# Kernel tuning notes

Hardware: AMD Instinct MI355X
Metric: run time of the kernel (lower is better)

## Reference

```python
import jax, jax.numpy as jnp
import numpy as np

N_LOC = 500000
N_CAT = 5000
N_EDGES = 2000000
LOC_DIM = 128
CAT_DIM = 128
INITRANGE = 0.1
NEG_SLOPE = 0.2


def setup_inputs() -> dict:
    key = jax.random.key(0)
    k1, k2, k3, k4 = jax.random.split(key, 4)
    loc_emb = jax.random.normal(k1, (N_LOC, LOC_DIM), dtype=jnp.float32)
    # loc_to_cat Linear params, init per init_weights(): uniform(-0.1, 0.1) weight, zero bias
    W = jax.random.uniform(k2, (CAT_DIM, LOC_DIM), dtype=jnp.float32,
                           minval=-INITRANGE, maxval=INITRANGE)
    b = jnp.zeros((CAT_DIM,), dtype=jnp.float32)
    edge_src = jax.random.randint(k3, (N_EDGES,), 0, N_LOC, dtype=jnp.int64)
    edge_dst = jax.random.randint(k4, (N_EDGES,), 0, N_CAT, dtype=jnp.int64)
    return {"loc_emb": loc_emb, "W": W, "b": b,
            "edge_src": edge_src, "edge_dst": edge_dst}


def reference(loc_emb, W, b, edge_src, edge_dst):
    # copy_u('f','m') + sum('m','in') across all canonical etypes, combined with 'sum':
    # gather source (loc) features along edges, segment-sum into cat nodes.
    msg = loc_emb[edge_src]                                   # [E, loc_dim]
    agg = jax.ops.segment_sum(msg, edge_dst, num_segments=N_CAT)  # [n_cat, loc_dim]
    # loc_to_cat linear + LeakyReLU(0.2)
    cat_emb = jax.nn.leaky_relu(agg @ W.T + b, negative_slope=NEG_SLOPE)
    return cat_emb
```

## Files before the change

### kernel.cpp

```cpp
#include <hip/hip_runtime.h>

#define N_LOC   500000
#define N_CAT   5000
#define N_EDGES 2000000
#define DIM     128
#define NEG_SLOPE 0.2f
#define PAD     5008
#define NB      256
#define EPB     ((N_EDGES + NB - 1) / NB)


__launch_bounds__(1024)
__global__ void blockhist_kernel(const int* __restrict__ edst, int* __restrict__ rank,
                                 int* __restrict__ bhist) {
    __shared__ int lh[N_CAT];
    int b = blockIdx.x, t = threadIdx.x;
    for (int c = t; c < N_CAT; c += 1024) lh[c] = 0;
    __syncthreads();
    int s = b * EPB;
    int e = min(s + EPB, N_EDGES);
    for (int i = s + t; i < e; i += 1024)
        rank[i] = atomicAdd(&lh[edst[i]], 1);
    __syncthreads();
    for (int c = t; c < N_CAT; c += 1024)
        bhist[(size_t)b * N_CAT + c] = lh[c];
}

__launch_bounds__(256)
__global__ void blockscan_kernel(int* __restrict__ bhist, int* __restrict__ tot) {
    int c = blockIdx.x * 256 + threadIdx.x;
    if (c >= N_CAT) return;
    int run = 0;
    for (int b0 = 0; b0 < NB; b0 += 8) {
        int v0 = bhist[(size_t)(b0 + 0) * N_CAT + c];
        int v1 = bhist[(size_t)(b0 + 1) * N_CAT + c];
        int v2 = bhist[(size_t)(b0 + 2) * N_CAT + c];
        int v3 = bhist[(size_t)(b0 + 3) * N_CAT + c];
        int v4 = bhist[(size_t)(b0 + 4) * N_CAT + c];
        int v5 = bhist[(size_t)(b0 + 5) * N_CAT + c];
        int v6 = bhist[(size_t)(b0 + 6) * N_CAT + c];
        int v7 = bhist[(size_t)(b0 + 7) * N_CAT + c];
        bhist[(size_t)(b0 + 0) * N_CAT + c] = run; run += v0;
        bhist[(size_t)(b0 + 1) * N_CAT + c] = run; run += v1;
        bhist[(size_t)(b0 + 2) * N_CAT + c] = run; run += v2;
        bhist[(size_t)(b0 + 3) * N_CAT + c] = run; run += v3;
        bhist[(size_t)(b0 + 4) * N_CAT + c] = run; run += v4;
        bhist[(size_t)(b0 + 5) * N_CAT + c] = run; run += v5;
        bhist[(size_t)(b0 + 6) * N_CAT + c] = run; run += v6;
        bhist[(size_t)(b0 + 7) * N_CAT + c] = run; run += v7;
    }
    tot[c] = run;
}

__launch_bounds__(1024)
__global__ void scan_kernel(const int* __restrict__ cnt, int* __restrict__ offsets) {
    __shared__ int wsum[16];
    __shared__ int woff[16];
    __shared__ int total_s;
    __shared__ int running_s;
    int t = threadIdx.x;
    int lane = t & 63, w = t >> 6;
    if (t == 0) { running_s = 0; offsets[0] = 0; }
    __syncthreads();
    for (int base = 0; base < N_CAT; base += 1024) {
        int i = base + t;
        int v = (i < N_CAT) ? cnt[i] : 0;
        int incl = v;
        #pragma unroll
        for (int off = 1; off < 64; off <<= 1) {
            int x = __shfl_up(incl, off, 64);
            if (lane >= off) incl += x;
        }
        if (lane == 63) wsum[w] = incl;
        __syncthreads();
        if (w == 0 && lane < 16) {
            int s = wsum[lane];
            int e = s;
            #pragma unroll
            for (int off = 1; off < 16; off <<= 1) {
                int x = __shfl_up(e, off, 64);
                if (lane >= off) e += x;
            }
            woff[lane] = e - s;
            if (lane == 15) total_s = e;
        }
        __syncthreads();
        int run = running_s;
        if (i < N_CAT) offsets[i + 1] = run + woff[w] + incl;
        __syncthreads();
        if (t == 0) running_s = run + total_s;
        __syncthreads();
    }
}

__global__ void fill2_kernel(const int* __restrict__ esrc, const int* __restrict__ edst,
                             const int* __restrict__ rank, const int* __restrict__ offsets,
                             const int* __restrict__ bhist, int* __restrict__ csr_src) {
    int i = blockIdx.x * blockDim.x + threadIdx.x;
    if (i < N_EDGES) {
        int c = edst[i];
        int b = i / EPB;
        csr_src[offsets[c] + bhist[(size_t)b * N_CAT + c] + rank[i]] = esrc[i];
    }
}

__global__ void transpose_kernel(const float* __restrict__ W, float* __restrict__ WT) {
    int j = blockIdx.x;
    int k = threadIdx.x;
    WT[k * DIM + j] = W[j * DIM + k];
}

__launch_bounds__(256)
__global__ void agg_fused_kernel(const float* __restrict__ loc, const int* __restrict__ csr_src,
                                 const int* __restrict__ offsets, const float* __restrict__ WT,
                                 const float* __restrict__ bias, float* __restrict__ out) {
    __shared__ float4 sacc[256];
    __shared__ float  srow[DIM];
    int c = blockIdx.x;
    int t = threadIdx.x;
    int g = t >> 5;
    int l = t & 31;
    int beg = offsets[c];
    int end = offsets[c + 1];
    int cnt = end - beg;
    int per = (cnt + 7) >> 3;
    int gbeg = beg + g * per;
    int gend = min(gbeg + per, end);

    float4 a0 = make_float4(0.f, 0.f, 0.f, 0.f);
    float4 a1 = make_float4(0.f, 0.f, 0.f, 0.f);
    float4 a2 = make_float4(0.f, 0.f, 0.f, 0.f);
    float4 a3 = make_float4(0.f, 0.f, 0.f, 0.f);
    int e = gbeg;
    for (; e + 4 <= gend; e += 4) {
        int s0 = csr_src[e + 0];
        int s1 = csr_src[e + 1];
        int s2 = csr_src[e + 2];
        int s3 = csr_src[e + 3];
        float4 v0 = ((const float4*)(loc + (size_t)s0 * DIM))[l];
        float4 v1 = ((const float4*)(loc + (size_t)s1 * DIM))[l];
        float4 v2 = ((const float4*)(loc + (size_t)s2 * DIM))[l];
        float4 v3 = ((const float4*)(loc + (size_t)s3 * DIM))[l];
        a0.x += v0.x; a0.y += v0.y; a0.z += v0.z; a0.w += v0.w;
        a1.x += v1.x; a1.y += v1.y; a1.z += v1.z; a1.w += v1.w;
        a2.x += v2.x; a2.y += v2.y; a2.z += v2.z; a2.w += v2.w;
        a3.x += v3.x; a3.y += v3.y; a3.z += v3.z; a3.w += v3.w;
    }
    for (; e < gend; ++e) {
        int s = csr_src[e];
        float4 v = ((const float4*)(loc + (size_t)s * DIM))[l];
        a0.x += v.x; a0.y += v.y; a0.z += v.z; a0.w += v.w;
    }
    float4 acc = make_float4((a0.x + a1.x) + (a2.x + a3.x),
                             (a0.y + a1.y) + (a2.y + a3.y),
                             (a0.z + a1.z) + (a2.z + a3.z),
                             (a0.w + a1.w) + (a2.w + a3.w));
    sacc[t] = acc;
    __syncthreads();
    if (t < 128) {
        float4 a = sacc[t], b = sacc[t + 128];
        sacc[t] = make_float4(a.x + b.x, a.y + b.y, a.z + b.z, a.w + b.w);
    }
    __syncthreads();
    if (t < 64) {
        float4 a = sacc[t], b = sacc[t + 64];
        sacc[t] = make_float4(a.x + b.x, a.y + b.y, a.z + b.z, a.w + b.w);
    }
    __syncthreads();
    if (t < 32) {
        float4 a = sacc[t], b = sacc[t + 32];
        srow[4 * t + 0] = a.x + b.x;
        srow[4 * t + 1] = a.y + b.y;
        srow[4 * t + 2] = a.z + b.z;
        srow[4 * t + 3] = a.w + b.w;
    }
    __syncthreads();
    int j = t & 127;
    int h = t >> 7;
    float m0 = 0.f, m1 = 0.f, m2 = 0.f, m3 = 0.f;
    int k0 = h * 64;
    #pragma unroll 4
    for (int k = 0; k < 64; k += 4) {
        m0 += WT[(k0 + k + 0) * DIM + j] * srow[k0 + k + 0];
        m1 += WT[(k0 + k + 1) * DIM + j] * srow[k0 + k + 1];
        m2 += WT[(k0 + k + 2) * DIM + j] * srow[k0 + k + 2];
        m3 += WT[(k0 + k + 3) * DIM + j] * srow[k0 + k + 3];
    }
    float* sred = (float*)sacc;
    sred[t] = (m0 + m1) + (m2 + m3);
    __syncthreads();
    if (t < 128) {
        float v = sred[t] + sred[t + 128] + bias[t];
        v = v > 0.f ? v : NEG_SLOPE * v;
        out[(size_t)c * DIM + t] = v;
    }
}


__global__ void hist_rank_kernel(const int* __restrict__ dst, int* __restrict__ cnt,
                                 int* __restrict__ rank, int n) {
    int i = blockIdx.x * blockDim.x + threadIdx.x;
    if (i < n) rank[i] = atomicAdd(&cnt[dst[i]], 1);
}

__global__ void fill_rank_kernel(const int* __restrict__ src, const int* __restrict__ dst,
                                 const int* __restrict__ rank, const int* __restrict__ offsets,
                                 int* __restrict__ csr_src, int n) {
    int i = blockIdx.x * blockDim.x + threadIdx.x;
    if (i < n) csr_src[offsets[dst[i]] + rank[i]] = src[i];
}

__global__ void zero_kernel(float* p, int n) {
    int i = blockIdx.x * blockDim.x + threadIdx.x;
    if (i < n) p[i] = 0.f;
}

__launch_bounds__(128)
__global__ void scatter_atomic_kernel(const float* __restrict__ loc, const int* __restrict__ src,
                                      const int* __restrict__ dst, float* __restrict__ agg) {
    int e = blockIdx.x;
    int d = threadIdx.x;
    int s = src[e];
    int c = dst[e];
    atomicAdd(&agg[(size_t)c * DIM + d], loc[(size_t)s * DIM + d]);
}

#define CATS_PER_BLOCK 8
__launch_bounds__(256)
__global__ void gemm_lrelu_kernel(const float* __restrict__ agg, const float* __restrict__ W,
                                  const float* __restrict__ b, float* __restrict__ out) {
    __shared__ float sW[DIM * 129];
    __shared__ float sA[CATS_PER_BLOCK * DIM];
    int t = threadIdx.x;
    int cbase = blockIdx.x * CATS_PER_BLOCK;
    for (int i = t; i < DIM * DIM; i += 256) {
        int j = i >> 7, k = i & 127;
        sW[j * 129 + k] = W[i];
    }
    for (int i = t; i < CATS_PER_BLOCK * DIM; i += 256) {
        sA[i] = agg[(size_t)cbase * DIM + i];
    }
    __syncthreads();
    int j = t & 127;
    int cc = t >> 7;
    float acc0 = 0.f, acc1 = 0.f, acc2 = 0.f, acc3 = 0.f;
    for (int k = 0; k < DIM; ++k) {
        float w = sW[j * 129 + k];
        acc0 += w * sA[(cc + 0) * DIM + k];
        acc1 += w * sA[(cc + 2) * DIM + k];
        acc2 += w * sA[(cc + 4) * DIM + k];
        acc3 += w * sA[(cc + 6) * DIM + k];
    }
    float bj = b[j];
    float r0 = acc0 + bj, r1 = acc1 + bj, r2 = acc2 + bj, r3 = acc3 + bj;
    r0 = r0 > 0.f ? r0 : NEG_SLOPE * r0;
    r1 = r1 > 0.f ? r1 : NEG_SLOPE * r1;
    r2 = r2 > 0.f ? r2 : NEG_SLOPE * r2;
    r3 = r3 > 0.f ? r3 : NEG_SLOPE * r3;
    out[(size_t)(cbase + cc + 0) * DIM + j] = r0;
    out[(size_t)(cbase + cc + 2) * DIM + j] = r1;
    out[(size_t)(cbase + cc + 4) * DIM + j] = r2;
    out[(size_t)(cbase + cc + 6) * DIM + j] = r3;
}

extern "C" void kernel_launch(void* const* d_in, const int* in_sizes, int n_in,
                              void* d_out, int out_size, void* d_ws, size_t ws_size,
                              hipStream_t stream) {
    const float* loc  = (const float*)d_in[0];
    const float* W    = (const float*)d_in[1];
    const float* bias = (const float*)d_in[2];
    const int*   esrc = (const int*)d_in[3];
    const int*   edst = (const int*)d_in[4];
    float* out = (float*)d_out;

    const int threads = 256;
    const int eblocks = (N_EDGES + threads - 1) / threads;

    size_t need_cs   = ((size_t)2 * N_EDGES + (size_t)NB * N_CAT + 2 * PAD + DIM * DIM) * sizeof(int);
    size_t need_rank = ((size_t)2 * N_EDGES + 2 * PAD + DIM * DIM) * sizeof(int);

    if (ws_size >= need_cs) {
        int*   rank    = (int*)d_ws;
        int*   csr_src = rank + N_EDGES;
        int*   bhist   = csr_src + N_EDGES;
        int*   tot     = bhist + (size_t)NB * N_CAT;
        int*   offsets = tot + PAD;
        float* WT      = (float*)(offsets + PAD);

        transpose_kernel<<<DIM, DIM, 0, stream>>>(W, WT);
        blockhist_kernel<<<NB, 1024, 0, stream>>>(edst, rank, bhist);
        blockscan_kernel<<<(N_CAT + 255) / 256, 256, 0, stream>>>(bhist, tot);
        scan_kernel<<<1, 1024, 0, stream>>>(tot, offsets);
        fill2_kernel<<<eblocks, threads, 0, stream>>>(esrc, edst, rank, offsets, bhist, csr_src);
        agg_fused_kernel<<<N_CAT, 256, 0, stream>>>(loc, csr_src, offsets, WT, bias, out);
    } else if (ws_size >= need_rank) {
        int* counts  = (int*)d_ws;
        int* offsets = counts + PAD;
        float* WT    = (float*)(offsets + PAD);
        int* rank    = (int*)(WT + DIM * DIM);
        int* csr_src = rank + N_EDGES;

        hipMemsetAsync(counts, 0, (size_t)PAD * sizeof(int), stream);
        transpose_kernel<<<DIM, DIM, 0, stream>>>(W, WT);
        hist_rank_kernel<<<eblocks, threads, 0, stream>>>(edst, counts, rank, N_EDGES);
        scan_kernel<<<1, 1024, 0, stream>>>(counts, offsets);
        fill_rank_kernel<<<eblocks, threads, 0, stream>>>(esrc, edst, rank, offsets, csr_src, N_EDGES);
        agg_fused_kernel<<<N_CAT, 256, 0, stream>>>(loc, csr_src, offsets, WT, bias, out);
    } else {
        int n = N_CAT * DIM;
        zero_kernel<<<(n + 255) / 256, 256, 0, stream>>>(out, n);
        scatter_atomic_kernel<<<N_EDGES, DIM, 0, stream>>>(loc, esrc, edst, out);
        gemm_lrelu_kernel<<<N_CAT / CATS_PER_BLOCK, 256, 0, stream>>>(out, W, bias, out);
    }
}
```

Baseline: 504.1 us.

## Fold weight transpose into histogram kernel, vectorize edge passes, deepen gather unroll

```diff
diff --git a/kernel.cpp b/kernel.cpp
--- a/kernel.cpp
+++ b/kernel.cpp
@@ -6,21 +6,40 @@
 #define DIM     128
 #define NEG_SLOPE 0.2f
 #define PAD     5008
-#define NB      256
-#define EPB     ((N_EDGES + NB - 1) / NB)
-
+#define NB      128
+#define EPB     15628
 
 __launch_bounds__(1024)
-__global__ void blockhist_kernel(const int* __restrict__ edst, int* __restrict__ rank,
+__global__ void blockhist_kernel(const int* __restrict__ edst, const float* __restrict__ W,
+                                 float* __restrict__ WT, int* __restrict__ rank,
                                  int* __restrict__ bhist) {
+    int b = blockIdx.x, t = threadIdx.x;
+    if (b == NB) {
+        for (int i = t; i < DIM * DIM; i += 1024) {
+            int j = i >> 7, k = i & 127;
+            WT[k * DIM + j] = W[j * DIM + k];
+        }
+        return;
+    }
     __shared__ int lh[N_CAT];
-    int b = blockIdx.x, t = threadIdx.x;
     for (int c = t; c < N_CAT; c += 1024) lh[c] = 0;
     __syncthreads();
     int s = b * EPB;
     int e = min(s + EPB, N_EDGES);
-    for (int i = s + t; i < e; i += 1024)
-        rank[i] = atomicAdd(&lh[edst[i]], 1);
+    int i = s + 4 * t;
+    for (; i + 4 <= e; i += 4096) {
+        int4 d = *(const int4*)(edst + i);
+        int4 r;
+        r.x = atomicAdd(&lh[d.x], 1);
+        r.y = atomicAdd(&lh[d.y], 1);
+        r.z = atomicAdd(&lh[d.z], 1);
+        r.w = atomicAdd(&lh[d.w], 1);
+        *(int4*)(rank + i) = r;
+    }
+    if (i < e) {
+        int lim = min(i + 4, e);
+        for (int j = i; j < lim; ++j) rank[j] = atomicAdd(&lh[edst[j]], 1);
+    }
     __syncthreads();
     for (int c = t; c < N_CAT; c += 1024)
         bhist[(size_t)b * N_CAT + c] = lh[c];
@@ -56,8 +75,7 @@
 __global__ void scan_kernel(const int* __restrict__ cnt, int* __restrict__ offsets) {
     __shared__ int wsum[16];
     __shared__ int woff[16];
-    __shared__ int total_s;
-    __shared__ int running_s;
+    __shared__ int total_s, running_s;
     int t = threadIdx.x;
     int lane = t & 63, w = t >> 6;
     if (t == 0) { running_s = 0; offsets[0] = 0; }
@@ -96,18 +114,23 @@
 __global__ void fill2_kernel(const int* __restrict__ esrc, const int* __restrict__ edst,
                              const int* __restrict__ rank, const int* __restrict__ offsets,
                              const int* __restrict__ bhist, int* __restrict__ csr_src) {
-    int i = blockIdx.x * blockDim.x + threadIdx.x;
-    if (i < N_EDGES) {
-        int c = edst[i];
-        int b = i / EPB;
-        csr_src[offsets[c] + bhist[(size_t)b * N_CAT + c] + rank[i]] = esrc[i];
-    }
-}
-
-__global__ void transpose_kernel(const float* __restrict__ W, float* __restrict__ WT) {
-    int j = blockIdx.x;
-    int k = threadIdx.x;
-    WT[k * DIM + j] = W[j * DIM + k];
+    int i4 = (blockIdx.x * blockDim.x + threadIdx.x) * 4;
+    if (i4 + 4 <= N_EDGES) {
+        int4 c = *(const int4*)(edst + i4);
+        int4 s = *(const int4*)(esrc + i4);
+        int4 r = *(const int4*)(rank + i4);
+        size_t bb = (size_t)(i4 / EPB) * N_CAT;
+        csr_src[offsets[c.x] + bhist[bb + c.x] + r.x] = s.x;
+        csr_src[offsets[c.y] + bhist[bb + c.y] + r.y] = s.y;
+        csr_src[offsets[c.z] + bhist[bb + c.z] + r.z] = s.z;
+        csr_src[offsets[c.w] + bhist[bb + c.w] + r.w] = s.w;
+    } else {
+        for (int i = i4; i < N_EDGES; ++i) {
+            int c = edst[i];
+            size_t bb = (size_t)(i / EPB) * N_CAT;
+            csr_src[offsets[c] + bhist[bb + c] + rank[i]] = esrc[i];
+        }
+    }
 }
 
 __launch_bounds__(256)
@@ -132,11 +155,28 @@
     float4 a2 = make_float4(0.f, 0.f, 0.f, 0.f);
     float4 a3 = make_float4(0.f, 0.f, 0.f, 0.f);
     int e = gbeg;
+    for (; e + 8 <= gend; e += 8) {
+        int s0 = csr_src[e + 0], s1 = csr_src[e + 1], s2 = csr_src[e + 2], s3 = csr_src[e + 3];
+        int s4 = csr_src[e + 4], s5 = csr_src[e + 5], s6 = csr_src[e + 6], s7 = csr_src[e + 7];
+        float4 v0 = ((const float4*)(loc + (size_t)s0 * DIM))[l];
+        float4 v1 = ((const float4*)(loc + (size_t)s1 * DIM))[l];
+        float4 v2 = ((const float4*)(loc + (size_t)s2 * DIM))[l];
+        float4 v3 = ((const float4*)(loc + (size_t)s3 * DIM))[l];
+        float4 v4 = ((const float4*)(loc + (size_t)s4 * DIM))[l];
+        float4 v5 = ((const float4*)(loc + (size_t)s5 * DIM))[l];
+        float4 v6 = ((const float4*)(loc + (size_t)s6 * DIM))[l];
+        float4 v7 = ((const float4*)(loc + (size_t)s7 * DIM))[l];
+        a0.x += v0.x; a0.y += v0.y; a0.z += v0.z; a0.w += v0.w;
+        a1.x += v1.x; a1.y += v1.y; a1.z += v1.z; a1.w += v1.w;
+        a2.x += v2.x; a2.y += v2.y; a2.z += v2.z; a2.w += v2.w;
+        a3.x += v3.x; a3.y += v3.y; a3.z += v3.z; a3.w += v3.w;
+        a0.x += v4.x; a0.y += v4.y; a0.z += v4.z; a0.w += v4.w;
+        a1.x += v5.x; a1.y += v5.y; a1.z += v5.z; a1.w += v5.w;
+        a2.x += v6.x; a2.y += v6.y; a2.z += v6.z; a2.w += v6.w;
+        a3.x += v7.x; a3.y += v7.y; a3.z += v7.z; a3.w += v7.w;
+    }
     for (; e + 4 <= gend; e += 4) {
-        int s0 = csr_src[e + 0];
-        int s1 = csr_src[e + 1];
-        int s2 = csr_src[e + 2];
-        int s3 = csr_src[e + 3];
+        int s0 = csr_src[e + 0], s1 = csr_src[e + 1], s2 = csr_src[e + 2], s3 = csr_src[e + 3];
         float4 v0 = ((const float4*)(loc + (size_t)s0 * DIM))[l];
         float4 v1 = ((const float4*)(loc + (size_t)s1 * DIM))[l];
         float4 v2 = ((const float4*)(loc + (size_t)s2 * DIM))[l];
@@ -210,6 +250,12 @@
     if (i < n) csr_src[offsets[dst[i]] + rank[i]] = src[i];
 }
 
+__global__ void transpose_kernel(const float* __restrict__ W, float* __restrict__ WT) {
+    int j = blockIdx.x;
+    int k = threadIdx.x;
+    WT[k * DIM + j] = W[j * DIM + k];
+}
+
 __global__ void zero_kernel(float* p, int n) {
     int i = blockIdx.x * blockDim.x + threadIdx.x;
     if (i < n) p[i] = 0.f;
@@ -220,9 +266,7 @@
                                       const int* __restrict__ dst, float* __restrict__ agg) {
     int e = blockIdx.x;
     int d = threadIdx.x;
-    int s = src[e];
-    int c = dst[e];
-    atomicAdd(&agg[(size_t)c * DIM + d], loc[(size_t)s * DIM + d]);
+    atomicAdd(&agg[(size_t)dst[e] * DIM + d], loc[(size_t)src[e] * DIM + d]);
 }
 
 #define CATS_PER_BLOCK 8
@@ -237,9 +281,8 @@
         int j = i >> 7, k = i & 127;
         sW[j * 129 + k] = W[i];
     }
-    for (int i = t; i < CATS_PER_BLOCK * DIM; i += 256) {
+    for (int i = t; i < CATS_PER_BLOCK * DIM; i += 256)
         sA[i] = agg[(size_t)cbase * DIM + i];
-    }
     __syncthreads();
     int j = t & 127;
     int cc = t >> 7;
@@ -273,10 +316,7 @@
     const int*   edst = (const int*)d_in[4];
     float* out = (float*)d_out;
 
-    const int threads = 256;
-    const int eblocks = (N_EDGES + threads - 1) / threads;
-
-    size_t need_cs   = ((size_t)2 * N_EDGES + (size_t)NB * N_CAT + 2 * PAD + DIM * DIM) * sizeof(int);
+    size_t need_cs   = ((size_t)2 * N_EDGES + (size_t)NB * N_CAT + 3 * PAD + DIM * DIM) * sizeof(int);
     size_t need_rank = ((size_t)2 * N_EDGES + 2 * PAD + DIM * DIM) * sizeof(int);
 
     if (ws_size >= need_cs) {
@@ -287,11 +327,10 @@
         int*   offsets = tot + PAD;
         float* WT      = (float*)(offsets + PAD);
 
-        transpose_kernel<<<DIM, DIM, 0, stream>>>(W, WT);
-        blockhist_kernel<<<NB, 1024, 0, stream>>>(edst, rank, bhist);
+        blockhist_kernel<<<NB + 1, 1024, 0, stream>>>(edst, W, WT, rank, bhist);
         blockscan_kernel<<<(N_CAT + 255) / 256, 256, 0, stream>>>(bhist, tot);
         scan_kernel<<<1, 1024, 0, stream>>>(tot, offsets);
-        fill2_kernel<<<eblocks, threads, 0, stream>>>(esrc, edst, rank, offsets, bhist, csr_src);
+        fill2_kernel<<<(N_EDGES / 4 + 255) / 256, 256, 0, stream>>>(esrc, edst, rank, offsets, bhist, csr_src);
         agg_fused_kernel<<<N_CAT, 256, 0, stream>>>(loc, csr_src, offsets, WT, bias, out);
     } else if (ws_size >= need_rank) {
         int* counts  = (int*)d_ws;
@@ -302,9 +341,10 @@
 
         hipMemsetAsync(counts, 0, (size_t)PAD * sizeof(int), stream);
         transpose_kernel<<<DIM, DIM, 0, stream>>>(W, WT);
-        hist_rank_kernel<<<eblocks, threads, 0, stream>>>(edst, counts, rank, N_EDGES);
+        const int eblocks = (N_EDGES + 255) / 256;
+        hist_rank_kernel<<<eblocks, 256, 0, stream>>>(edst, counts, rank, N_EDGES);
         scan_kernel<<<1, 1024, 0, stream>>>(counts, offsets);
-        fill_rank_kernel<<<eblocks, threads, 0, stream>>>(esrc, edst, rank, offsets, csr_src, N_EDGES);
+        fill_rank_kernel<<<eblocks, 256, 0, stream>>>(esrc, edst, rank, offsets, csr_src, N_EDGES);
         agg_fused_kernel<<<N_CAT, 256, 0, stream>>>(loc, csr_src, offsets, WT, bias, out);
     } else {
         int n = N_CAT * DIM;
```

Measured after the change: 493.4 us. 1.02x faster.
